# Performance work log

Measured on AMD Instinct MI355X. Metric: run time of the kernel, lower is better.

The kernel has to match this reference:

```python
import jax, jax.numpy as jnp
import numpy as np


def _haar_kernel():
    # 8 orthonormal 3D Haar taps, order (zf,yf,xf) in {L,H}^3 -> subband index s=4*z+2*y+x
    s2 = np.sqrt(2.0)
    L = np.array([1.0, 1.0]) / s2
    H = np.array([1.0, -1.0]) / s2
    taps = []
    for zf in (L, H):
        for yf in (L, H):
            for xf in (L, H):
                taps.append(np.einsum('i,j,k->ijk', zf, yf, xf))
    return jnp.asarray(np.stack(taps, 0), dtype=jnp.float32)  # [8,2,2,2]


def setup_inputs() -> dict:
    key = jax.random.key(0)
    ks = jax.random.split(key, 9)
    C, mid = 128, 8  # channels=128, reduction=16 -> mid = max(1, 128//16)
    x = jax.random.normal(ks[0], (2, C, 64, 64, 64), jnp.float32)
    def p(k, shape):
        return jax.random.normal(k, shape, jnp.float32) * 0.05
    return {
        'x': x,
        'gw1': p(ks[1], (mid, C)), 'gb1': p(ks[2], (mid,)),
        'gw2': p(ks[3], (C, mid)), 'gb2': p(ks[4], (C,)),
        'lw1': p(ks[5], (mid, C)), 'lb1': p(ks[6], (mid,)),
        'lw2': p(ks[7], (C, mid)), 'lb2': p(ks[8], (C,)),
    }


def _mlp(t, w1, b1, w2, b2):
    # 1x1x1 Conv3d -> ReLU -> 1x1x1 Conv3d, t: [B,C,D,H,W]
    h = jnp.einsum('bcdhw,mc->bmdhw', t, w1) + b1[None, :, None, None, None]
    h = jax.nn.relu(h)
    return jnp.einsum('bmdhw,cm->bcdhw', h, w2) + b2[None, :, None, None, None]


def reference(x, gw1, gb1, gw2, gb2, lw1, lb1, lw2, lb2):
    k = _haar_kernel()  # [8,2,2,2]
    B, C, D, H, W = x.shape
    # depthwise stride-2 2x2x2 conv == non-overlapping block transform
    xr = x.reshape(B, C, D // 2, 2, H // 2, 2, W // 2, 2)
    y = jnp.einsum('bcdphqwr,spqr->bcsdhw', xr, k)  # [B,C,8,D/2,H/2,W/2]
    low = y[:, :, 0]        # [B,C,D/2,H/2,W/2]
    highs = y[:, :, 1:]     # [B,C,7,D/2,H/2,W/2]
    x_sum = low + highs.sum(axis=2)
    gap = x_sum.mean(axis=(2, 3, 4), keepdims=True)  # AdaptiveAvgPool3d(1)
    w = jax.nn.sigmoid(_mlp(gap, gw1, gb1, gw2, gb2) + _mlp(x_sum, lw1, lb1, lw2, lb2))
    y_mod = jnp.concatenate([low[:, :, None], highs * w[:, :, None]], axis=2)
    # conv_transpose of orthonormal Haar == inverse block transform
    xr2 = jnp.einsum('bcsdhw,spqr->bcdphqwr', y_mod, k)
    return xr2.reshape(B, C, D, H, W)
```

## Files before the change

### kernel.cpp

```cpp
#include <hip/hip_runtime.h>
#include <math.h>

#define C_ 128
#define MID 8
#define CS 262144
#define SQRT8 2.8284271247461903f

static __device__ __forceinline__ float sigmoidf_(float z) {
    return 1.0f / (1.0f + __expf(-z));
}

__global__ __launch_bounds__(256) void corner_kernel(
    const float* __restrict__ x,
    const float* __restrict__ lw1, const float* __restrict__ lb1,
    const float* __restrict__ lw2, const float* __restrict__ lb2,
    float* __restrict__ partial,
    float* __restrict__ lout)
{
    __shared__ float xs[C_ * 33];
    __shared__ float hid[MID * 32];
    __shared__ float slw1[MID * C_];
    __shared__ float slw2[C_ * MID];

    const int blk = blockIdx.x;
    const int b  = blk >> 10;
    const int dc = (blk >> 5) & 31;
    const int hc = blk & 31;
    const int tid = threadIdx.x;

    for (int i = tid; i < MID * C_; i += 256) slw1[i] = lw1[i];
    for (int i = tid; i < C_ * MID; i += 256) slw2[i] = lw2[i];

    const float* xb = x + (size_t)b * C_ * CS + (size_t)(((2 * dc) * 64 + 2 * hc) * 64);
    const int f = tid & 15;
    {
        int c = tid >> 4;
        #pragma unroll
        for (int k = 0; k < 8; ++k, c += 16) {
            float4 v = ((const float4*)(xb + (size_t)c * CS))[f];
            xs[c * 33 + 2 * f]     = SQRT8 * v.x;
            xs[c * 33 + 2 * f + 1] = SQRT8 * v.z;
            float sc = v.x + v.z;
            sc += __shfl_down(sc, 8);
            sc += __shfl_down(sc, 4);
            sc += __shfl_down(sc, 2);
            sc += __shfl_down(sc, 1);
            if (f == 0) partial[blk * C_ + c] = sc;
        }
    }
    __syncthreads();

    {
        int m = tid >> 5, wc = tid & 31;
        float a = lb1[m];
        for (int cc = 0; cc < C_; ++cc) a += slw1[m * C_ + cc] * xs[cc * 33 + wc];
        hid[m * 32 + wc] = fmaxf(a, 0.0f);
    }
    __syncthreads();

    {
        int wc = tid & 31, c0 = tid >> 5;
        float hv[MID];
        #pragma unroll
        for (int m = 0; m < MID; ++m) hv[m] = hid[m * 32 + wc];
        float* lo = lout + (size_t)blk * (C_ * 32);
        #pragma unroll
        for (int i = 0; i < 16; ++i) {
            int cc = c0 * 16 + i;
            float a = lb2[cc];
            #pragma unroll
            for (int m = 0; m < MID; ++m) a += slw2[cc * MID + m] * hv[m];
            lo[cc * 32 + wc] = a;
        }
    }
}

__global__ __launch_bounds__(1024) void gmlp_kernel(
    const float* __restrict__ partial,
    const float* __restrict__ gw1, const float* __restrict__ gb1,
    const float* __restrict__ gw2, const float* __restrict__ gb2,
    float* __restrict__ gout)
{
    __shared__ float red[8][C_];
    __shared__ float sgap[C_];
    __shared__ float shid[MID];
    const int b = blockIdx.x;
    const int t = threadIdx.x;
    const int c = t & 127, chunk = t >> 7;
    float s = 0.0f;
    const float* p = partial + (size_t)(b * 1024 + chunk * 128) * C_ + c;
    for (int j = 0; j < 128; ++j) s += p[(size_t)j * C_];
    red[chunk][c] = s;
    __syncthreads();
    if (t < C_) {
        float tot = 0.0f;
        #pragma unroll
        for (int k = 0; k < 8; ++k) tot += red[k][c];
        sgap[c] = tot * (SQRT8 / 32768.0f);
    }
    __syncthreads();
    if (t < MID) {
        float a = gb1[t];
        for (int cc = 0; cc < C_; ++cc) a += gw1[t * C_ + cc] * sgap[cc];
        shid[t] = fmaxf(a, 0.0f);
    }
    __syncthreads();
    if (t < C_) {
        float a = gb2[t];
        #pragma unroll
        for (int m = 0; m < MID; ++m) a += gw2[t * MID + m] * shid[m];
        gout[b * C_ + t] = a;
    }
}

__global__ __launch_bounds__(256) void blend_kernel(
    const float* __restrict__ x,
    const float* __restrict__ lout,
    const float* __restrict__ gout,
    float* __restrict__ out)
{
    const int blk  = blockIdx.x;
    const int half = blk & 1;
    const int dc   = (blk >> 1) & 31;
    const int c    = (blk >> 6) & 127;
    const int b    = blk >> 13;
    const int tid  = threadIdx.x;
    const int f    = tid & 15;
    const int hc   = half * 16 + (tid >> 4);

    const size_t off = (size_t)(b * C_ + c) * CS
                     + (size_t)(2 * dc) * 4096 + (size_t)(2 * hc) * 64;
    float4 a00 = ((const float4*)(x + off))[f];
    float4 a01 = ((const float4*)(x + off + 64))[f];
    float4 a10 = ((const float4*)(x + off + 4096))[f];
    float4 a11 = ((const float4*)(x + off + 4160))[f];

    const float go = gout[b * C_ + c];
    const float2 g2 = *(const float2*)(lout
        + ((size_t)(((b * 32 + dc) * 32 + hc) * C_ + c)) * 32 + 2 * f);
    const float w0 = sigmoidf_(g2.x + go);
    const float w1 = sigmoidf_(g2.y + go);
    const float mean0 = (a00.x + a00.y + a01.x + a01.y +
                         a10.x + a10.y + a11.x + a11.y) * 0.125f;
    const float mean1 = (a00.z + a00.w + a01.z + a01.w +
                         a10.z + a10.w + a11.z + a11.w) * 0.125f;
    const float om0 = (1.0f - w0) * mean0;
    const float om1 = (1.0f - w1) * mean1;

    float4 o;
    o.x = w0 * a00.x + om0; o.y = w0 * a00.y + om0;
    o.z = w1 * a00.z + om1; o.w = w1 * a00.w + om1;
    ((float4*)(out + off))[f] = o;
    o.x = w0 * a01.x + om0; o.y = w0 * a01.y + om0;
    o.z = w1 * a01.z + om1; o.w = w1 * a01.w + om1;
    ((float4*)(out + off + 64))[f] = o;
    o.x = w0 * a10.x + om0; o.y = w0 * a10.y + om0;
    o.z = w1 * a10.z + om1; o.w = w1 * a10.w + om1;
    ((float4*)(out + off + 4096))[f] = o;
    o.x = w0 * a11.x + om0; o.y = w0 * a11.y + om0;
    o.z = w1 * a11.z + om1; o.w = w1 * a11.w + om1;
    ((float4*)(out + off + 4160))[f] = o;
}

extern "C" void kernel_launch(void* const* d_in, const int* in_sizes, int n_in,
                              void* d_out, int out_size, void* d_ws, size_t ws_size,
                              hipStream_t stream) {
    const float* x   = (const float*)d_in[0];
    const float* gw1 = (const float*)d_in[1];
    const float* gb1 = (const float*)d_in[2];
    const float* gw2 = (const float*)d_in[3];
    const float* gb2 = (const float*)d_in[4];
    const float* lw1 = (const float*)d_in[5];
    const float* lb1 = (const float*)d_in[6];
    const float* lw2 = (const float*)d_in[7];
    const float* lb2 = (const float*)d_in[8];
    float* o  = (float*)d_out;
    float* ws = (float*)d_ws;

    float* partial = ws;
    float* gout    = ws + 262144;
    float* lout    = ws + 262400;

    corner_kernel<<<2048, 256, 0, stream>>>(x, lw1, lb1, lw2, lb2, partial, lout);
    gmlp_kernel<<<2, 1024, 0, stream>>>(partial, gw1, gb1, gw2, gb2, gout);
    blend_kernel<<<16384, 256, 0, stream>>>(x, lout, gout, o);
}
```

Measured before the change: 487.0 us.

## Fuse local MLP into blend kernel and drop lout intermediate buffer

The local MLP (second layer and sigmoid) moves into the blend kernel, so the large per-position lout intermediate is no longer written and re-read. The GAP partial sum becomes its own per-channel reduction kernel that reads only corner samples. The global MLP now runs in one block and folds lb2 into a combined bias. Each blend block recomputes the first MLP layer from its corner samples, and each block's reads span 128 channel strides, which may lower memory locality.

Result: no change. 480.7 us (-1.3%).

```diff
diff --git a/kernel.cpp b/kernel.cpp
--- a/kernel.cpp
+++ b/kernel.cpp
@@ -10,156 +10,163 @@
     return 1.0f / (1.0f + __expf(-z));
 }
 
-__global__ __launch_bounds__(256) void corner_kernel(
+__global__ __launch_bounds__(256) void gap_partial_kernel(
+    const float* __restrict__ x,
+    float* __restrict__ partial)
+{
+    __shared__ float red[4];
+    const int blk = blockIdx.x;
+    const int g = blk & 7;
+    const int c = (blk >> 3) & 127;
+    const int b = blk >> 10;
+    const int tid = threadIdx.x;
+    const int f = tid & 15;
+
+    const float* xb = x + (size_t)(b * C_ + c) * CS;
+    float s = 0.0f;
+    #pragma unroll
+    for (int k = 0; k < 8; ++k) {
+        const int r   = (tid >> 4) + 16 * k;
+        const int dcl = r >> 5;
+        const int hc  = r & 31;
+        const float4 v = ((const float4*)(
+            xb + (size_t)(2 * (4 * g + dcl)) * 4096 + (size_t)(2 * hc) * 64))[f];
+        s += v.x + v.z;
+    }
+    s += __shfl_down(s, 32);
+    s += __shfl_down(s, 16);
+    s += __shfl_down(s, 8);
+    s += __shfl_down(s, 4);
+    s += __shfl_down(s, 2);
+    s += __shfl_down(s, 1);
+    if ((tid & 63) == 0) red[tid >> 6] = s;
+    __syncthreads();
+    if (tid == 0) partial[blk] = red[0] + red[1] + red[2] + red[3];
+}
+
+__global__ __launch_bounds__(256) void gmlp_kernel(
+    const float* __restrict__ partial,
+    const float* __restrict__ gw1, const float* __restrict__ gb1,
+    const float* __restrict__ gw2, const float* __restrict__ gb2,
+    const float* __restrict__ lb2,
+    float* __restrict__ gbias)
+{
+    __shared__ float sgap[2][C_];
+    __shared__ float shid[2][MID];
+    const int t = threadIdx.x;
+    const int b = t >> 7, c = t & 127;
+    {
+        const float4* p = (const float4*)(partial + (size_t)t * 8);
+        const float4 a = p[0], d = p[1];
+        sgap[b][c] = (a.x + a.y + a.z + a.w + d.x + d.y + d.z + d.w)
+                     * (SQRT8 / 32768.0f);
+    }
+    __syncthreads();
+    if (t < 16) {
+        const int bb = t >> 3, m = t & 7;
+        float a = gb1[m];
+        for (int cc = 0; cc < C_; ++cc) a += gw1[m * C_ + cc] * sgap[bb][cc];
+        shid[bb][m] = fmaxf(a, 0.0f);
+    }
+    __syncthreads();
+    float a = gb2[c] + lb2[c];
+    #pragma unroll
+    for (int m = 0; m < MID; ++m) a += gw2[c * MID + m] * shid[b][m];
+    gbias[t] = a;
+}
+
+__global__ __launch_bounds__(256) void fused_blend_kernel(
     const float* __restrict__ x,
     const float* __restrict__ lw1, const float* __restrict__ lb1,
-    const float* __restrict__ lw2, const float* __restrict__ lb2,
-    float* __restrict__ partial,
-    float* __restrict__ lout)
+    const float* __restrict__ lw2,
+    const float* __restrict__ gbias,
+    float* __restrict__ out)
 {
-    __shared__ float xs[C_ * 33];
-    __shared__ float hid[MID * 32];
-    __shared__ float slw1[MID * C_];
-    __shared__ float slw2[C_ * MID];
+    __shared__ float xs[C_ * 17];
+    __shared__ float shid[MID * 16];
+    __shared__ float s1T[C_ * MID];
+    __shared__ float s2T[MID * C_];
+    __shared__ float sgb[C_];
 
     const int blk = blockIdx.x;
-    const int b  = blk >> 10;
-    const int dc = (blk >> 5) & 31;
-    const int hc = blk & 31;
+    const int wh  = blk & 1;
+    const int hc  = (blk >> 1) & 31;
+    const int dc  = (blk >> 6) & 31;
+    const int b   = blk >> 11;
     const int tid = threadIdx.x;
+    const int f   = tid & 7;
+    const int c0  = tid >> 3;
 
-    for (int i = tid; i < MID * C_; i += 256) slw1[i] = lw1[i];
-    for (int i = tid; i < C_ * MID; i += 256) slw2[i] = lw2[i];
+    for (int i = tid; i < MID * C_; i += 256) {
+        s1T[i] = lw1[(i & 7) * C_ + (i >> 3)];
+        s2T[i] = lw2[(i & 127) * MID + (i >> 7)];
+    }
+    if (tid < C_) sgb[tid] = gbias[b * C_ + tid];
 
-    const float* xb = x + (size_t)b * C_ * CS + (size_t)(((2 * dc) * 64 + 2 * hc) * 64);
-    const int f = tid & 15;
-    {
-        int c = tid >> 4;
-        #pragma unroll
-        for (int k = 0; k < 8; ++k, c += 16) {
-            float4 v = ((const float4*)(xb + (size_t)c * CS))[f];
-            xs[c * 33 + 2 * f]     = SQRT8 * v.x;
-            xs[c * 33 + 2 * f + 1] = SQRT8 * v.z;
-            float sc = v.x + v.z;
-            sc += __shfl_down(sc, 8);
-            sc += __shfl_down(sc, 4);
-            sc += __shfl_down(sc, 2);
-            sc += __shfl_down(sc, 1);
-            if (f == 0) partial[blk * C_ + c] = sc;
-        }
+    const float* xb = x + (size_t)b * C_ * CS
+                    + (size_t)(2 * dc) * 4096 + (size_t)(2 * hc) * 64 + wh * 32;
+
+    float4 r00[4];
+    #pragma unroll
+    for (int k = 0; k < 4; ++k) {
+        const int c = c0 + 32 * k;
+        const float4 v = ((const float4*)(xb + (size_t)c * CS))[f];
+        r00[k] = v;
+        xs[c * 17 + 2 * f]     = SQRT8 * v.x;
+        xs[c * 17 + 2 * f + 1] = SQRT8 * v.z;
     }
     __syncthreads();
 
-    {
-        int m = tid >> 5, wc = tid & 31;
+    if (tid < 128) {
+        const int m = tid >> 4, wc = tid & 15;
         float a = lb1[m];
-        for (int cc = 0; cc < C_; ++cc) a += slw1[m * C_ + cc] * xs[cc * 33 + wc];
-        hid[m * 32 + wc] = fmaxf(a, 0.0f);
+        for (int cc = 0; cc < C_; ++cc) a += s1T[cc * MID + m] * xs[cc * 17 + wc];
+        shid[m * 16 + wc] = fmaxf(a, 0.0f);
     }
     __syncthreads();
 
-    {
-        int wc = tid & 31, c0 = tid >> 5;
-        float hv[MID];
+    float* ob = out + (xb - x);
+    #pragma unroll
+    for (int k = 0; k < 4; ++k) {
+        const int c = c0 + 32 * k;
+        const size_t coff = (size_t)c * CS;
+
+        const float4 a01 = ((const float4*)(xb + coff + 64))[f];
+        const float4 a10 = ((const float4*)(xb + coff + 4096))[f];
+        const float4 a11 = ((const float4*)(xb + coff + 4160))[f];
+        const float4 a00 = r00[k];
+
+        float d0 = sgb[c], d1 = sgb[c];
         #pragma unroll
-        for (int m = 0; m < MID; ++m) hv[m] = hid[m * 32 + wc];
-        float* lo = lout + (size_t)blk * (C_ * 32);
-        #pragma unroll
-        for (int i = 0; i < 16; ++i) {
-            int cc = c0 * 16 + i;
-            float a = lb2[cc];
-            #pragma unroll
-            for (int m = 0; m < MID; ++m) a += slw2[cc * MID + m] * hv[m];
-            lo[cc * 32 + wc] = a;
+        for (int m = 0; m < MID; ++m) {
+            const float wv = s2T[m * C_ + c];
+            d0 += wv * shid[m * 16 + 2 * f];
+            d1 += wv * shid[m * 16 + 2 * f + 1];
         }
+        const float w0 = sigmoidf_(d0);
+        const float w1 = sigmoidf_(d1);
+
+        const float mean0 = (a00.x + a00.y + a01.x + a01.y +
+                             a10.x + a10.y + a11.x + a11.y) * 0.125f;
+        const float mean1 = (a00.z + a00.w + a01.z + a01.w +
+                             a10.z + a10.w + a11.z + a11.w) * 0.125f;
+        const float om0 = (1.0f - w0) * mean0;
+        const float om1 = (1.0f - w1) * mean1;
+
+        float4 o;
+        o.x = w0 * a00.x + om0; o.y = w0 * a00.y + om0;
+        o.z = w1 * a00.z + om1; o.w = w1 * a00.w + om1;
+        ((float4*)(ob + coff))[f] = o;
+        o.x = w0 * a01.x + om0; o.y = w0 * a01.y + om0;
+        o.z = w1 * a01.z + om1; o.w = w1 * a01.w + om1;
+        ((float4*)(ob + coff + 64))[f] = o;
+        o.x = w0 * a10.x + om0; o.y = w0 * a10.y + om0;
+        o.z = w1 * a10.z + om1; o.w = w1 * a10.w + om1;
+        ((float4*)(ob + coff + 4096))[f] = o;
+        o.x = w0 * a11.x + om0; o.y = w0 * a11.y + om0;
+        o.z = w1 * a11.z + om1; o.w = w1 * a11.w + om1;
+        ((float4*)(ob + coff + 4160))[f] = o;
     }
-}
-
-__global__ __launch_bounds__(1024) void gmlp_kernel(
-    const float* __restrict__ partial,
-    const float* __restrict__ gw1, const float* __restrict__ gb1,
-    const float* __restrict__ gw2, const float* __restrict__ gb2,
-    float* __restrict__ gout)
-{
-    __shared__ float red[8][C_];
-    __shared__ float sgap[C_];
-    __shared__ float shid[MID];
-    const int b = blockIdx.x;
-    const int t = threadIdx.x;
-    const int c = t & 127, chunk = t >> 7;
-    float s = 0.0f;
-    const float* p = partial + (size_t)(b * 1024 + chunk * 128) * C_ + c;
-    for (int j = 0; j < 128; ++j) s += p[(size_t)j * C_];
-    red[chunk][c] = s;
-    __syncthreads();
-    if (t < C_) {
-        float tot = 0.0f;
-        #pragma unroll
-        for (int k = 0; k < 8; ++k) tot += red[k][c];
-        sgap[c] = tot * (SQRT8 / 32768.0f);
-    }
-    __syncthreads();
-    if (t < MID) {
-        float a = gb1[t];
-        for (int cc = 0; cc < C_; ++cc) a += gw1[t * C_ + cc] * sgap[cc];
-        shid[t] = fmaxf(a, 0.0f);
-    }
-    __syncthreads();
-    if (t < C_) {
-        float a = gb2[t];
-        #pragma unroll
-        for (int m = 0; m < MID; ++m) a += gw2[t * MID + m] * shid[m];
-        gout[b * C_ + t] = a;
-    }
-}
-
-__global__ __launch_bounds__(256) void blend_kernel(
-    const float* __restrict__ x,
-    const float* __restrict__ lout,
-    const float* __restrict__ gout,
-    float* __restrict__ out)
-{
-    const int blk  = blockIdx.x;
-    const int half = blk & 1;
-    const int dc   = (blk >> 1) & 31;
-    const int c    = (blk >> 6) & 127;
-    const int b    = blk >> 13;
-    const int tid  = threadIdx.x;
-    const int f    = tid & 15;
-    const int hc   = half * 16 + (tid >> 4);
-
-    const size_t off = (size_t)(b * C_ + c) * CS
-                     + (size_t)(2 * dc) * 4096 + (size_t)(2 * hc) * 64;
-    float4 a00 = ((const float4*)(x + off))[f];
-    float4 a01 = ((const float4*)(x + off + 64))[f];
-    float4 a10 = ((const float4*)(x + off + 4096))[f];
-    float4 a11 = ((const float4*)(x + off + 4160))[f];
-
-    const float go = gout[b * C_ + c];
-    const float2 g2 = *(const float2*)(lout
-        + ((size_t)(((b * 32 + dc) * 32 + hc) * C_ + c)) * 32 + 2 * f);
-    const float w0 = sigmoidf_(g2.x + go);
-    const float w1 = sigmoidf_(g2.y + go);
-    const float mean0 = (a00.x + a00.y + a01.x + a01.y +
-                         a10.x + a10.y + a11.x + a11.y) * 0.125f;
-    const float mean1 = (a00.z + a00.w + a01.z + a01.w +
-                         a10.z + a10.w + a11.z + a11.w) * 0.125f;
-    const float om0 = (1.0f - w0) * mean0;
-    const float om1 = (1.0f - w1) * mean1;
-
-    float4 o;
-    o.x = w0 * a00.x + om0; o.y = w0 * a00.y + om0;
-    o.z = w1 * a00.z + om1; o.w = w1 * a00.w + om1;
-    ((float4*)(out + off))[f] = o;
-    o.x = w0 * a01.x + om0; o.y = w0 * a01.y + om0;
-    o.z = w1 * a01.z + om1; o.w = w1 * a01.w + om1;
-    ((float4*)(out + off + 64))[f] = o;
-    o.x = w0 * a10.x + om0; o.y = w0 * a10.y + om0;
-    o.z = w1 * a10.z + om1; o.w = w1 * a10.w + om1;
-    ((float4*)(out + off + 4096))[f] = o;
-    o.x = w0 * a11.x + om0; o.y = w0 * a11.y + om0;
-    o.z = w1 * a11.z + om1; o.w = w1 * a11.w + om1;
-    ((float4*)(out + off + 4160))[f] = o;
 }
 
 extern "C" void kernel_launch(void* const* d_in, const int* in_sizes, int n_in,
@@ -178,10 +185,9 @@
     float* ws = (float*)d_ws;
 
     float* partial = ws;
-    float* gout    = ws + 262144;
-    float* lout    = ws + 262400;
+    float* gbias   = ws + 2048;
 
-    corner_kernel<<<2048, 256, 0, stream>>>(x, lw1, lb1, lw2, lb2, partial, lout);
-    gmlp_kernel<<<2, 1024, 0, stream>>>(partial, gw1, gb1, gw2, gb2, gout);
-    blend_kernel<<<16384, 256, 0, stream>>>(x, lout, gout, o);
+    gap_partial_kernel<<<2048, 256, 0, stream>>>(x, partial);
+    gmlp_kernel<<<1, 256, 0, stream>>>(partial, gw1, gb1, gw2, gb2, lb2, gbias);
+    fused_blend_kernel<<<4096, 256, 0, stream>>>(x, lw1, lb1, lw2, gbias, o);
 }
```
